# Kernel tuning notes

Measured on AMD Instinct MI355X. Metric: run time of the kernel, lower is better.

## Reference

```python
import jax, jax.numpy as jnp
import numpy as np

EMB = 1024
HEADS = 16
HEAD_DIM = EMB // HEADS


def setup_inputs() -> dict:
    key = jax.random.key(0)
    ks = jax.random.split(key, 6)
    B, S = 4, 1024
    inputs = jax.random.normal(ks[0], (B, S, EMB), dtype=jnp.float32)
    # causal mask: 1.0 where attention is disallowed (added * -1e9 in the layer)
    mask = (1.0 - jnp.tril(jnp.ones((S, S), dtype=jnp.float32)))[None, None, :, :]
    scale = 1.0 / np.sqrt(EMB)
    wq = jax.random.normal(ks[1], (EMB, EMB), dtype=jnp.float32) * scale
    wk = jax.random.normal(ks[2], (EMB, EMB), dtype=jnp.float32) * scale
    wv = jax.random.normal(ks[3], (EMB, EMB), dtype=jnp.float32) * scale
    wo = jax.random.normal(ks[4], (EMB, EMB), dtype=jnp.float32) * scale
    zb = jnp.zeros((EMB,), dtype=jnp.float32)
    return {"inputs": inputs, "mask": mask, "wq": wq, "bq": zb, "wk": wk,
            "bk": zb, "wv": wv, "bv": zb, "wo": wo, "bo": zb}


def _split_heads(t, B):
    # [B, S, E] -> [B, H, S, Dh]
    return t.reshape(B, -1, HEADS, HEAD_DIM).transpose(0, 2, 1, 3)


def reference(inputs, mask, wq, bq, wk, bk, wv, bv, wo, bo):
    B = inputs.shape[0]
    q = _split_heads(inputs @ wq + bq, B)
    k = _split_heads(inputs @ wk + bk, B)
    v = _split_heads(inputs @ wv + bv, B)
    # NOTE: source divides by sqrt(sqrt(head_num)) = head_num**0.25
    scores = jnp.einsum('bhsd,bhtd->bhst', q, k) / jnp.asarray(HEADS, inputs.dtype) ** 0.25
    if mask is not None:
        scores = scores + mask * -1e9
    attn = jax.nn.softmax(scores, axis=-1)
    z = jnp.einsum('bhst,bhtd->bhsd', attn, v)
    # Faithful to source: reshape [B,H,S,Dh] -> [B,S,E] WITHOUT transposing heads back
    z = z.reshape(B, -1, EMB)
    return z @ wo + bo
```

## Files before the change

### kernel.cpp

```cpp
#include <hip/hip_runtime.h>
#include <hip/hip_bf16.h>
#include <stdint.h>

typedef __attribute__((ext_vector_type(8))) short short8;
typedef __attribute__((ext_vector_type(4))) float float4v;

#define SEQ   1024
#define NQKV  3072

__device__ __forceinline__ float bf2f(ushort h) {
    union { uint u; float f; } c; c.u = ((uint)h) << 16; return c.f;
}
__device__ __forceinline__ ushort f2bf(float f) {
    union { uint u; float f; } c; c.f = f;
    uint u = c.u;
    return (ushort)((u + 0x7fffu + ((u >> 16) & 1u)) >> 16);
}
__device__ __forceinline__ uint cvt_pk_bf16(float lo, float hi) {
    uint r;
    asm volatile("v_cvt_pk_bf16_f32 %0, %1, %2" : "=v"(r) : "v"(lo), "v"(hi));
    return r;
}
__device__ __forceinline__ void gl2lds16(const ushort* g, ushort* l) {
    __builtin_amdgcn_global_load_lds(
        (const __attribute__((address_space(1))) unsigned int*)(g),
        (__attribute__((address_space(3))) unsigned int*)(l),
        16, 0, 0);
}

__global__ __launch_bounds__(256) void prep_k(const void* __restrict__ X,
                                              const void* __restrict__ w0,
                                              const void* __restrict__ w1,
                                              const void* __restrict__ w2,
                                              const void* __restrict__ w3,
                                              const void* __restrict__ bq,
                                              const void* __restrict__ bk,
                                              const void* __restrict__ bv,
                                              const void* __restrict__ bo,
                                              ushort* __restrict__ xc,
                                              ushort* __restrict__ biasout,
                                              ushort* __restrict__ wtall,
                                              int* __restrict__ flag) {
    __shared__ int tot;
    __shared__ ushort tile[64][72];
    int t = threadIdx.x;
    if (t == 0) tot = 0;
    __syncthreads();
    uint wv = ((const uint*)X)[t];
    uint e = (wv >> 7) & 0xFFu;
    bool isbf = (e >= 100u && e <= 130u);
    unsigned long long m = __ballot(isbf);
    if ((t & 63) == 0) atomicAdd(&tot, __popcll(m));
    __syncthreads();
    bool isf = (tot <= 128);

    int bi = blockIdx.x;
    if (bi == 0 && t == 0) flag[0] = isf ? 1 : 0;

    if (bi < 4096) {
        if (!isf) return;
        int i = (bi * 256 + t) * 4;
        float4 v = *(const float4*)((const float*)X + i);
        ushort4 o;
        o.x = f2bf(v.x); o.y = f2bf(v.y); o.z = f2bf(v.z); o.w = f2bf(v.w);
        *(ushort4*)(xc + i) = o;
    } else if (bi < 4112) {
        int i = (bi - 4096) * 256 + t;
        int sel = i >> 10, j = i & 1023;
        const void* p = (sel == 0) ? bq : (sel == 1) ? bk : (sel == 2) ? bv : bo;
        biasout[i] = isf ? f2bf(((const float*)p)[j]) : ((const ushort*)p)[j];
    } else {
        int idx = bi - 4112;
        int z = idx >> 8, rem = idx & 255;
        const void* in = (z == 0) ? w0 : (z == 1) ? w1 : (z == 2) ? w2 : w3;
        ushort* out = wtall + (size_t)z * 1024 * 1024;
        int k0 = (rem & 15) * 64, n0 = (rem >> 4) * 64;
        int r = t >> 3, c = (t & 7) * 8;
#pragma unroll
        for (int p = 0; p < 2; p++) {
            int rr = r + p * 32;
            if (isf) {
                const float* src = (const float*)in + (size_t)(k0 + rr) * 1024 + n0 + c;
                float4 v0 = *(const float4*)src;
                float4 v1 = *(const float4*)(src + 4);
                tile[rr][c + 0] = f2bf(v0.x); tile[rr][c + 1] = f2bf(v0.y);
                tile[rr][c + 2] = f2bf(v0.z); tile[rr][c + 3] = f2bf(v0.w);
                tile[rr][c + 4] = f2bf(v1.x); tile[rr][c + 5] = f2bf(v1.y);
                tile[rr][c + 6] = f2bf(v1.z); tile[rr][c + 7] = f2bf(v1.w);
            } else {
                uint4 v = *(const uint4*)((const ushort*)in + (size_t)(k0 + rr) * 1024 + n0 + c);
                *(uint4*)&tile[rr][c] = v;
            }
        }
        __syncthreads();
#pragma unroll
        for (int p = 0; p < 2; p++) {
            int n = r + p * 32;
            ushort vals[8];
#pragma unroll
            for (int j = 0; j < 8; j++) vals[j] = tile[c + j][n];
            *(uint4*)(out + (size_t)(n0 + n) * 1024 + k0 + c) = *(uint4*)vals;
        }
    }
}

template <int BM, bool DUAL, bool WRV>
__global__ __launch_bounds__(256) void gemm_k(const ushort* __restrict__ Araw,
                                              const ushort* __restrict__ Aconv,
                                              const ushort* __restrict__ BT,
                                              const ushort* __restrict__ bias,
                                              void* __restrict__ C,
                                              ushort* __restrict__ vt,
                                              const int* __restrict__ flag,
                                              int M, int N, int K) {
    constexpr int RM = BM / 32;
    constexpr int AJ = BM / 64;
    __shared__ ushort As[2][BM * 32];
    __shared__ ushort Bs[2][128 * 32];
    int nwgx = gridDim.x;
    int orig = blockIdx.y * nwgx + blockIdx.x;
    int cpx = (nwgx * gridDim.y) >> 3;
    int swz = (orig & 7) * cpx + (orig >> 3);
    int n0 = (swz % nwgx) * 128, m0 = (swz / nwgx) * BM;
    int t = threadIdx.x;
    int w = t >> 6, lane = t & 63, q = lane >> 4, ln = lane & 15;
    int wr = w >> 1, wc = w & 1;
    const ushort* A = (*flag) ? Aconv : Araw;

    float4v acc[RM][4];
#pragma unroll
    for (int r = 0; r < RM; r++)
#pragma unroll
        for (int cc = 0; cc < 4; cc++) acc[r][cc] = (float4v){0.f, 0.f, 0.f, 0.f};

#pragma unroll
    for (int j = 0; j < AJ; j++) {
        int c = j * 256 + t;
        int row = c >> 2, s = c & 3;
        int kc = s ^ ((row >> 1) & 3);
        gl2lds16(A + (size_t)(m0 + row) * K + kc * 8, &As[0][c * 8]);
    }
#pragma unroll
    for (int j = 0; j < 2; j++) {
        int c = j * 256 + t;
        int row = c >> 2, s = c & 3;
        int kc = s ^ ((row >> 1) & 3);
        gl2lds16(BT + (size_t)(n0 + row) * K + kc * 8, &Bs[0][c * 8]);
    }

    int nIter = K >> 5;
    for (int kt = 0; kt < nIter; kt++) {
        int cur = kt & 1;
        __syncthreads();
        if (kt + 1 < nIter) {
            int nk0 = (kt + 1) << 5, nxt = cur ^ 1;
#pragma unroll
            for (int j = 0; j < AJ; j++) {
                int c = j * 256 + t;
                int row = c >> 2, s = c & 3;
                int kc = s ^ ((row >> 1) & 3);
                gl2lds16(A + (size_t)(m0 + row) * K + nk0 + kc * 8, &As[nxt][c * 8]);
            }
#pragma unroll
            for (int j = 0; j < 2; j++) {
                int c = j * 256 + t;
                int row = c >> 2, s = c & 3;
                int kc = s ^ ((row >> 1) & 3);
                gl2lds16(BT + (size_t)(n0 + row) * K + nk0 + kc * 8, &Bs[nxt][c * 8]);
            }
        }
        short8 af[RM], bf[4];
#pragma unroll
        for (int r = 0; r < RM; r++) {
            int row = wr * (BM / 2) + r * 16 + ln;
            af[r] = *(const short8*)&As[cur][((row << 2) | (q ^ ((row >> 1) & 3))) * 8];
        }
#pragma unroll
        for (int cc = 0; cc < 4; cc++) {
            int col = wc * 64 + cc * 16 + ln;
            bf[cc] = *(const short8*)&Bs[cur][((col << 2) | (q ^ ((col >> 1) & 3))) * 8];
        }
#pragma unroll
        for (int r = 0; r < RM; r++)
#pragma unroll
            for (int cc = 0; cc < 4; cc++)
                acc[r][cc] = __builtin_amdgcn_mfma_f32_16x16x32_bf16(af[r], bf[cc], acc[r][cc], 0, 0, 0);
    }

    bool outf = DUAL && (*flag != 0);
    bool wrv = WRV && (n0 >= 2048);
#pragma unroll
    for (int cc = 0; cc < 4; cc++) {
        int n = n0 + wc * 64 + cc * 16 + ln;
        float bs = bf2f(bias[n]);
#pragma unroll
        for (int r = 0; r < RM; r++) {
            ushort pk[4];
#pragma unroll
            for (int i = 0; i < 4; i++) {
                int m = m0 + wr * (BM / 2) + r * 16 + q * 4 + i;
                float v = acc[r][cc][i] + bs;
                if (outf) ((float*)C)[(size_t)m * N + n] = v;
                else      ((ushort*)C)[(size_t)m * N + n] = f2bf(v);
                pk[i] = f2bf(v);
            }
            if (wrv) {
                int mb = m0 + wr * (BM / 2) + r * 16 + q * 4;
                int b = mb >> 10, trow = mb & 1023;
                int h = (n - 2048) >> 6, d = n & 63;
                *(ushort4*)(vt + (((size_t)(b * 16 + h) * 64 + d) * 1024 + trow)) = *(ushort4*)pk;
            }
        }
    }
}

__global__ __launch_bounds__(512) void attn_k(const ushort* __restrict__ qkv,
                                              const ushort* __restrict__ vt,
                                              ushort* __restrict__ zp) {
    __shared__ ushort Ks[2][64 * 64];
    __shared__ ushort Vs[2][64 * 64];
    __shared__ ushort P[8][16 * 76];
    int bh = blockIdx.y;
    int pr = (bh & 32) ? (7 - blockIdx.x) : blockIdx.x;
    int b = bh >> 4, h = bh & 15;
    int t = threadIdx.x;
    int w = t >> 6;
    int grp = w >> 2;
    int lane = t & 63, q = lane >> 4, ln = lane & 15;

    const float CE = 0.72134752f;

    const ushort* Qp = qkv + (size_t)(b * SEQ) * NQKV + h * 64;
    const ushort* Kp = qkv + (size_t)(b * SEQ) * NQKV + 1024 + h * 64;
    const ushort* Vt = vt + (size_t)bh * 64 * 1024;

    int row0 = t >> 3, kc0 = (t & 7) ^ (row0 & 7);

    int tiB = 15 - pr;
    int ti = grp ? tiB : pr;
    int sw = ti * 64 + (w & 3) * 16;

    short8 aq0 = *(const short8*)(Qp + (size_t)(sw + ln) * NQKV + q * 8);
    short8 aq1 = *(const short8*)(Qp + (size_t)(sw + ln) * NQKV + 32 + q * 8);

    float lp = 0.f;
    float4v o[4];
#pragma unroll
    for (int nb = 0; nb < 4; nb++) o[nb] = (float4v){0.f, 0.f, 0.f, 0.f};

    gl2lds16(Kp + (size_t)row0 * NQKV + kc0 * 8, &Ks[0][t * 8]);
    gl2lds16(Vt + (size_t)row0 * 1024 + kc0 * 8, &Vs[0][t * 8]);

    int srow_l = sw + ln;

    for (int kt = 0; kt <= tiB; kt++) {
        int cur = kt & 1;
        int t0 = kt * 64;
        __syncthreads();
        if (kt < tiB) {
            int nt0 = t0 + 64, nxt = cur ^ 1;
            gl2lds16(Kp + (size_t)(nt0 + row0) * NQKV + kc0 * 8, &Ks[nxt][t * 8]);
            gl2lds16(Vt + (size_t)row0 * 1024 + nt0 + kc0 * 8, &Vs[nxt][t * 8]);
        }
        if (kt <= ti) {
            float4v s[4];
#pragma unroll
            for (int nb = 0; nb < 4; nb++) {
                int row = nb * 16 + ln;
                short8 kf0 = *(const short8*)&Ks[cur][((row << 3) | (q ^ (row & 7))) * 8];
                short8 kf1 = *(const short8*)&Ks[cur][((row << 3) | ((4 + q) ^ (row & 7))) * 8];
                s[nb] = (float4v){0.f, 0.f, 0.f, 0.f};
                s[nb] = __builtin_amdgcn_mfma_f32_16x16x32_bf16(kf0, aq0, s[nb], 0, 0, 0);
                s[nb] = __builtin_amdgcn_mfma_f32_16x16x32_bf16(kf1, aq1, s[nb], 0, 0, 0);
            }
            float p[4][4];
            if (kt < ti) {
#pragma unroll
                for (int nb = 0; nb < 4; nb++)
#pragma unroll
                    for (int i = 0; i < 4; i++) p[nb][i] = exp2f(s[nb][i] * CE);
            } else {
#pragma unroll
                for (int nb = 0; nb < 4; nb++)
#pragma unroll
                    for (int i = 0; i < 4; i++) {
                        int tcol = t0 + nb * 16 + q * 4 + i;
                        p[nb][i] = exp2f((tcol <= srow_l) ? s[nb][i] * CE : -1e30f);
                    }
            }
#pragma unroll
            for (int nb = 0; nb < 4; nb++)
                lp += (p[nb][0] + p[nb][1]) + (p[nb][2] + p[nb][3]);
#pragma unroll
            for (int nb = 0; nb < 4; nb++) {
                uint2 pk;
                pk.x = cvt_pk_bf16(p[nb][0], p[nb][1]);
                pk.y = cvt_pk_bf16(p[nb][2], p[nb][3]);
                *(uint2*)&P[w][ln * 76 + nb * 16 + q * 4] = pk;
            }
            asm volatile("s_waitcnt lgkmcnt(0)\n" ::: "memory");
            short8 ap0 = *(const short8*)&P[w][ln * 76 + q * 8];
            short8 ap1 = *(const short8*)&P[w][ln * 76 + 32 + q * 8];
#pragma unroll
            for (int nb = 0; nb < 4; nb++) {
                int row = nb * 16 + ln;
                short8 bv0 = *(const short8*)&Vs[cur][((row << 3) | (q ^ (row & 7))) * 8];
                short8 bv1 = *(const short8*)&Vs[cur][((row << 3) | ((4 + q) ^ (row & 7))) * 8];
                o[nb] = __builtin_amdgcn_mfma_f32_16x16x32_bf16(ap0, bv0, o[nb], 0, 0, 0);
                o[nb] = __builtin_amdgcn_mfma_f32_16x16x32_bf16(ap1, bv1, o[nb], 0, 0, 0);
            }
        }
    }

    float lred = lp;
    lred += __shfl_xor(lred, 16, 64);
    lred += __shfl_xor(lred, 32, 64);
    float l_i[4];
#pragma unroll
    for (int i = 0; i < 4; i++)
        l_i[i] = __shfl(lred, (q << 4) | (q * 4 + i), 64);

#pragma unroll
    for (int nb = 0; nb < 4; nb++) {
#pragma unroll
        for (int i = 0; i < 4; i++) {
            int srow = sw + q * 4 + i;
            int d = nb * 16 + ln;
            float z = o[nb][i] / l_i[i];
            int sp = h * 64 + (srow >> 4);
            int ep = ((srow & 15) << 6) + d;
            zp[((size_t)(b * SEQ + sp)) * 1024 + ep] = f2bf(z);
        }
    }
}

extern "C" void kernel_launch(void* const* d_in, const int* in_sizes, int n_in,
                              void* d_out, int out_size, void* d_ws, size_t ws_size,
                              hipStream_t stream) {
    const void* X  = d_in[0];
    const void* wq = d_in[2];
    const void* bq = d_in[3];
    const void* wk = d_in[4];
    const void* bk = d_in[5];
    const void* wv = d_in[6];
    const void* bv = d_in[7];
    const void* wo = d_in[8];
    const void* bo = d_in[9];

    char* ws = (char*)d_ws;
    int*    flag  = (int*)ws;
    ushort* biasq = (ushort*)(ws + 4096);
    ushort* WTall = (ushort*)(ws + 12288);
    ushort* Xc    = (ushort*)(ws + 8400896);
    ushort* QKV   = (ushort*)(ws + 16789504);
    ushort* VT    = (ushort*)(ws + 41955328);
    ushort* WTo   = WTall + 3 * 1024 * 1024;
    ushort* ZP    = Xc;

    prep_k<<<5136, 256, 0, stream>>>(X, wq, wk, wv, wo, bq, bk, bv, bo,
                                     Xc, biasq, WTall, flag);
    gemm_k<128, false, true><<<dim3(24, 32), 256, 0, stream>>>(
        (const ushort*)X, Xc, WTall, biasq, QKV, VT, flag, 4096, NQKV, 1024);
    attn_k<<<dim3(8, 64), 512, 0, stream>>>(QKV, VT, ZP);
    gemm_k<64, true, false><<<dim3(8, 64), 256, 0, stream>>>(
        ZP, ZP, WTo, biasq + 3072, d_out, nullptr, flag, 4096, 1024, 1024);
}
```

Measured before the change: 181.9 us.

## Replace QKV projection GEMM with 256x256 tiled, ping-pong pipelined kernel

The QKV projection now uses a new 512-thread kernel that computes 256x256 output tiles with a 64-wide K step, XOR-swizzled LDS staging through direct global-to-LDS loads, and double buffering. Loads for the next K slice are interleaved between the four MFMA quadrants and separated by barriers. The aim is to raise arithmetic intensity per block and hide global memory latency behind the MFMAs. Only 192 blocks are launched, which may leave some compute units underused, and the large LDS and register footprint limits occupancy.

```diff
diff --git a/kernel.cpp b/kernel.cpp
--- a/kernel.cpp
+++ b/kernel.cpp
@@ -27,6 +27,9 @@
         (__attribute__((address_space(3))) unsigned int*)(l),
         16, 0, 0);
 }
+
+#define FENCE() asm volatile("" ::: "memory")
+#define PBAR()  do { FENCE(); __builtin_amdgcn_s_barrier(); FENCE(); } while (0)
 
 __global__ __launch_bounds__(256) void prep_k(const void* __restrict__ X,
                                               const void* __restrict__ w0,
@@ -104,6 +107,149 @@
     }
 }
 
+__device__ __forceinline__ void stage_half(const ushort* src, int K, ushort* lds, int t) {
+#pragma unroll
+    for (int jj = 0; jj < 2; jj++) {
+        int c = jj * 512 + t;
+        int row = c >> 3, s = c & 7;
+        int kc = s ^ (row & 7);
+        gl2lds16(src + (size_t)row * K + kc * 8, lds + c * 8);
+    }
+}
+
+__global__ __launch_bounds__(512, 2) void gemm256_k(const ushort* __restrict__ Araw,
+                                                    const ushort* __restrict__ Aconv,
+                                                    const ushort* __restrict__ BT,
+                                                    const ushort* __restrict__ bias,
+                                                    ushort* __restrict__ C,
+                                                    ushort* __restrict__ vt,
+                                                    const int* __restrict__ flag) {
+    constexpr int K = 1024;
+    constexpr int N = NQKV;
+    __shared__ ushort As[2][256 * 64];
+    __shared__ ushort Bs[2][256 * 64];
+    int orig = blockIdx.y * gridDim.x + blockIdx.x;
+    int swz = (orig & 7) * 24 + (orig >> 3);
+    int n0 = (swz % 12) * 256, m0 = (swz / 12) * 256;
+    int t = threadIdx.x;
+    int w = t >> 6, lane = t & 63, q = lane >> 4, ln = lane & 15;
+    int wr = w & 1, wc = w >> 1;
+    const ushort* A = (*flag) ? Aconv : Araw;
+
+    float4v acc[8][4];
+#pragma unroll
+    for (int r = 0; r < 8; r++)
+#pragma unroll
+        for (int cc = 0; cc < 4; cc++) acc[r][cc] = (float4v){0.f, 0.f, 0.f, 0.f};
+
+    stage_half(A  + (size_t)m0 * K,           K, &As[0][0], t);
+    stage_half(A  + (size_t)(m0 + 128) * K,   K, &As[0][128 * 64], t);
+    stage_half(BT + (size_t)n0 * K,           K, &Bs[0][0], t);
+    stage_half(BT + (size_t)(n0 + 128) * K,   K, &Bs[0][128 * 64], t);
+    stage_half(A  + (size_t)m0 * K + 64,      K, &As[1][0], t);
+    stage_half(A  + (size_t)(m0 + 128) * K + 64, K, &As[1][128 * 64], t);
+    asm volatile("s_waitcnt vmcnt(4)" ::: "memory");
+    PBAR();
+
+    short8 af[4][2];
+    short8 bf[2][2][2];
+
+    for (int j = 0; j < 16; j++) {
+        int cur = j & 1;
+        int nxt = cur ^ 1;
+#pragma unroll
+        for (int mf = 0; mf < 4; mf++)
+#pragma unroll
+            for (int kh = 0; kh < 2; kh++) {
+                int r = wr * 64 + mf * 16 + ln;
+                af[mf][kh] = *(const short8*)&As[cur][(r * 8 + ((kh * 4 + q) ^ (r & 7))) * 8];
+            }
+#pragma unroll
+        for (int nf = 0; nf < 2; nf++)
+#pragma unroll
+            for (int kh = 0; kh < 2; kh++) {
+                int rb = wc * 64 + nf * 16 + ln;
+                bf[0][nf][kh] = *(const short8*)&Bs[cur][(rb * 8 + ((kh * 4 + q) ^ (rb & 7))) * 8];
+            }
+        if (j + 1 < 16) stage_half(BT + (size_t)n0 * K + (j + 1) * 64, K, &Bs[nxt][0], t);
+#pragma unroll
+        for (int mf = 0; mf < 4; mf++)
+#pragma unroll
+            for (int nf = 0; nf < 2; nf++)
+#pragma unroll
+                for (int kh = 0; kh < 2; kh++)
+                    acc[mf][nf] = __builtin_amdgcn_mfma_f32_16x16x32_bf16(af[mf][kh], bf[0][nf][kh], acc[mf][nf], 0, 0, 0);
+        PBAR();
+#pragma unroll
+        for (int nf = 0; nf < 2; nf++)
+#pragma unroll
+            for (int kh = 0; kh < 2; kh++) {
+                int rb = wc * 64 + 32 + nf * 16 + ln;
+                bf[1][nf][kh] = *(const short8*)&Bs[cur][(rb * 8 + ((kh * 4 + q) ^ (rb & 7))) * 8];
+            }
+        if (j + 1 < 16) stage_half(BT + (size_t)(n0 + 128) * K + (j + 1) * 64, K, &Bs[nxt][128 * 64], t);
+#pragma unroll
+        for (int mf = 0; mf < 4; mf++)
+#pragma unroll
+            for (int nf = 0; nf < 2; nf++)
+#pragma unroll
+                for (int kh = 0; kh < 2; kh++)
+                    acc[mf][2 + nf] = __builtin_amdgcn_mfma_f32_16x16x32_bf16(af[mf][kh], bf[1][nf][kh], acc[mf][2 + nf], 0, 0, 0);
+        PBAR();
+#pragma unroll
+        for (int mf = 0; mf < 4; mf++)
+#pragma unroll
+            for (int kh = 0; kh < 2; kh++) {
+                int r = 128 + wr * 64 + mf * 16 + ln;
+                af[mf][kh] = *(const short8*)&As[cur][(r * 8 + ((kh * 4 + q) ^ (r & 7))) * 8];
+            }
+        if (j + 2 < 16) stage_half(A + (size_t)m0 * K + (j + 2) * 64, K, &As[cur][0], t);
+#pragma unroll
+        for (int mf = 0; mf < 4; mf++)
+#pragma unroll
+            for (int nf = 0; nf < 2; nf++)
+#pragma unroll
+                for (int kh = 0; kh < 2; kh++)
+                    acc[4 + mf][2 + nf] = __builtin_amdgcn_mfma_f32_16x16x32_bf16(af[mf][kh], bf[1][nf][kh], acc[4 + mf][2 + nf], 0, 0, 0);
+        PBAR();
+        if (j + 2 < 16) stage_half(A + (size_t)(m0 + 128) * K + (j + 2) * 64, K, &As[cur][128 * 64], t);
+#pragma unroll
+        for (int mf = 0; mf < 4; mf++)
+#pragma unroll
+            for (int nf = 0; nf < 2; nf++)
+#pragma unroll
+                for (int kh = 0; kh < 2; kh++)
+                    acc[4 + mf][nf] = __builtin_amdgcn_mfma_f32_16x16x32_bf16(af[mf][kh], bf[0][nf][kh], acc[4 + mf][nf], 0, 0, 0);
+        if (j < 14) { asm volatile("s_waitcnt vmcnt(4)" ::: "memory"); }
+        else        { asm volatile("s_waitcnt vmcnt(0)" ::: "memory"); }
+        PBAR();
+    }
+
+    bool wrv = (n0 >= 2048);
+#pragma unroll
+    for (int nfull = 0; nfull < 4; nfull++) {
+        int n = n0 + wc * 64 + nfull * 16 + ln;
+        float bs = bf2f(bias[n]);
+#pragma unroll
+        for (int m8 = 0; m8 < 8; m8++) {
+            ushort pk[4];
+#pragma unroll
+            for (int i = 0; i < 4; i++) {
+                int m = m0 + (m8 >> 2) * 128 + wr * 64 + (m8 & 3) * 16 + q * 4 + i;
+                float v = acc[m8][nfull][i] + bs;
+                C[(size_t)m * N + n] = f2bf(v);
+                pk[i] = f2bf(v);
+            }
+            if (wrv) {
+                int mb = m0 + (m8 >> 2) * 128 + wr * 64 + (m8 & 3) * 16 + q * 4;
+                int b = mb >> 10, trow = mb & 1023;
+                int h = (n - 2048) >> 6, d = n & 63;
+                *(ushort4*)(vt + (((size_t)(b * 16 + h) * 64 + d) * 1024 + trow)) = *(ushort4*)pk;
+            }
+        }
+    }
+}
+
 template <int BM, bool DUAL, bool WRV>
 __global__ __launch_bounds__(256) void gemm_k(const ushort* __restrict__ Araw,
                                               const ushort* __restrict__ Aconv,
@@ -359,8 +505,8 @@
 
     prep_k<<<5136, 256, 0, stream>>>(X, wq, wk, wv, wo, bq, bk, bv, bo,
                                      Xc, biasq, WTall, flag);
-    gemm_k<128, false, true><<<dim3(24, 32), 256, 0, stream>>>(
-        (const ushort*)X, Xc, WTall, biasq, QKV, VT, flag, 4096, NQKV, 1024);
+    gemm256_k<<<dim3(12, 16), 512, 0, stream>>>(
+        (const ushort*)X, Xc, WTall, biasq, QKV, VT, flag);
     attn_k<<<dim3(8, 64), 512, 0, stream>>>(QKV, VT, ZP);
     gemm_k<64, true, false><<<dim3(8, 64), 256, 0, stream>>>(
         ZP, ZP, WTo, biasq + 3072, d_out, nullptr, flag, 4096, 1024, 1024);
```

Result: no change. 184.5 us (+1.5%).

## Triple-buffer GEMM LDS loads with explicit vmcnt waits and raw barrier

Applied to the files above, without the earlier changes.

Moves the GEMM K-loop from a double-buffered to a three-stage LDS ring. Global-to-LDS prefetch now runs two tiles ahead. The full __syncthreads is replaced by a partial s_waitcnt vmcnt(4) plus s_barrier, so the loads for the newest stage can stay in flight while the current tile is computed. This costs extra LDS, which may lower occupancy. The hardcoded vmcnt count matches only the configuration with four loads per stage, so it could be wrong for other BM instantiations.

```diff
diff --git a/kernel.cpp b/kernel.cpp
--- a/kernel.cpp
+++ b/kernel.cpp
@@ -27,6 +27,8 @@
         (__attribute__((address_space(3))) unsigned int*)(l),
         16, 0, 0);
 }
+
+#define FENCE() asm volatile("" ::: "memory")
 
 __global__ __launch_bounds__(256) void prep_k(const void* __restrict__ X,
                                               const void* __restrict__ w0,
@@ -115,8 +117,10 @@
                                               int M, int N, int K) {
     constexpr int RM = BM / 32;
     constexpr int AJ = BM / 64;
-    __shared__ ushort As[2][BM * 32];
-    __shared__ ushort Bs[2][128 * 32];
+    constexpr int ASZ = BM * 32;
+    constexpr int BSZ = 128 * 32;
+    __shared__ ushort As[3 * ASZ];
+    __shared__ ushort Bs[3 * BSZ];
     int nwgx = gridDim.x;
     int orig = blockIdx.y * nwgx + blockIdx.x;
     int cpx = (nwgx * gridDim.y) >> 3;
@@ -133,58 +137,71 @@
 #pragma unroll
         for (int cc = 0; cc < 4; cc++) acc[r][cc] = (float4v){0.f, 0.f, 0.f, 0.f};
 
-#pragma unroll
-    for (int j = 0; j < AJ; j++) {
-        int c = j * 256 + t;
-        int row = c >> 2, s = c & 3;
-        int kc = s ^ ((row >> 1) & 3);
-        gl2lds16(A + (size_t)(m0 + row) * K + kc * 8, &As[0][c * 8]);
-    }
-#pragma unroll
-    for (int j = 0; j < 2; j++) {
-        int c = j * 256 + t;
-        int row = c >> 2, s = c & 3;
-        int kc = s ^ ((row >> 1) & 3);
-        gl2lds16(BT + (size_t)(n0 + row) * K + kc * 8, &Bs[0][c * 8]);
-    }
-
     int nIter = K >> 5;
+
+#pragma unroll
+    for (int pj = 0; pj < 2; pj++) {
+        int jk0 = pj << 5;
+#pragma unroll
+        for (int j = 0; j < AJ; j++) {
+            int c = j * 256 + t;
+            int row = c >> 2, s = c & 3;
+            int kc = s ^ ((row >> 1) & 3);
+            gl2lds16(A + (size_t)(m0 + row) * K + jk0 + kc * 8, &As[pj * ASZ + c * 8]);
+        }
+#pragma unroll
+        for (int j = 0; j < 2; j++) {
+            int c = j * 256 + t;
+            int row = c >> 2, s = c & 3;
+            int kc = s ^ ((row >> 1) & 3);
+            gl2lds16(BT + (size_t)(n0 + row) * K + jk0 + kc * 8, &Bs[pj * BSZ + c * 8]);
+        }
+    }
+
+    int cur = 0;
+    int stg = 2;
     for (int kt = 0; kt < nIter; kt++) {
-        int cur = kt & 1;
-        __syncthreads();
-        if (kt + 1 < nIter) {
-            int nk0 = (kt + 1) << 5, nxt = cur ^ 1;
+        if (kt + 1 < nIter) { asm volatile("s_waitcnt vmcnt(4)" ::: "memory"); }
+        else                { asm volatile("s_waitcnt vmcnt(0)" ::: "memory"); }
+        FENCE();
+        __builtin_amdgcn_s_barrier();
+        FENCE();
+        __builtin_amdgcn_sched_barrier(0);
+        if (kt + 2 < nIter) {
+            int nk0 = (kt + 2) << 5;
 #pragma unroll
             for (int j = 0; j < AJ; j++) {
                 int c = j * 256 + t;
                 int row = c >> 2, s = c & 3;
                 int kc = s ^ ((row >> 1) & 3);
-                gl2lds16(A + (size_t)(m0 + row) * K + nk0 + kc * 8, &As[nxt][c * 8]);
+                gl2lds16(A + (size_t)(m0 + row) * K + nk0 + kc * 8, &As[stg * ASZ + c * 8]);
             }
 #pragma unroll
             for (int j = 0; j < 2; j++) {
                 int c = j * 256 + t;
                 int row = c >> 2, s = c & 3;
                 int kc = s ^ ((row >> 1) & 3);
-                gl2lds16(BT + (size_t)(n0 + row) * K + nk0 + kc * 8, &Bs[nxt][c * 8]);
+                gl2lds16(BT + (size_t)(n0 + row) * K + nk0 + kc * 8, &Bs[stg * BSZ + c * 8]);
             }
         }
         short8 af[RM], bf[4];
 #pragma unroll
         for (int r = 0; r < RM; r++) {
             int row = wr * (BM / 2) + r * 16 + ln;
-            af[r] = *(const short8*)&As[cur][((row << 2) | (q ^ ((row >> 1) & 3))) * 8];
+            af[r] = *(const short8*)&As[cur * ASZ + ((row << 2) | (q ^ ((row >> 1) & 3))) * 8];
         }
 #pragma unroll
         for (int cc = 0; cc < 4; cc++) {
             int col = wc * 64 + cc * 16 + ln;
-            bf[cc] = *(const short8*)&Bs[cur][((col << 2) | (q ^ ((col >> 1) & 3))) * 8];
+            bf[cc] = *(const short8*)&Bs[cur * BSZ + ((col << 2) | (q ^ ((col >> 1) & 3))) * 8];
         }
 #pragma unroll
         for (int r = 0; r < RM; r++)
 #pragma unroll
             for (int cc = 0; cc < 4; cc++)
                 acc[r][cc] = __builtin_amdgcn_mfma_f32_16x16x32_bf16(af[r], bf[cc], acc[r][cc], 0, 0, 0);
+        cur = (cur == 2) ? 0 : cur + 1;
+        stg = (stg == 2) ? 0 : stg + 1;
     }
 
     bool outf = DUAL && (*flag != 0);
```

Result: no change. 180.5 us (-0.8%).
